# Kernel tuning notes

Hardware: AMD Instinct MI355X
Metric: run time of the kernel (lower is better)

Reference implementation:

```python
import jax, jax.numpy as jnp
import numpy as np

R = 32
EPS = 0.0
BN_EPS = 1e-5


def _voxelize(features, idx):
    # features: [C, N], idx: [N] int32 flat voxel index in [0, R^3)
    V = R * R * R
    pts = features.T  # [N, C]
    sums = jax.ops.segment_sum(pts, idx, num_segments=V)          # [V, C]
    cnts = jax.ops.segment_sum(jnp.ones_like(idx, jnp.float32), idx, num_segments=V)  # [V]
    avg = sums / jnp.maximum(cnts, 1.0)[:, None]
    mx = jax.ops.segment_max(pts, idx, num_segments=V)            # [V, C], -inf for empty
    mx = jnp.where(cnts[:, None] > 0, mx, 0.0)
    return avg, mx, cnts


def reference(features, coords, conv_w, conv_b, bn_gamma, bn_beta, bn_mean, bn_var):
    B, C, N = features.shape
    # --- coordinate normalization (coords detached in original) ---
    nc = coords - jnp.mean(coords, axis=2, keepdims=True)          # [B,3,N]
    norms = jnp.linalg.norm(nc, axis=1, keepdims=True)             # [B,1,N]
    denom = jnp.max(norms, axis=2, keepdims=True) * 2.0 + EPS      # [B,1,1]
    nc = nc / denom + 0.5
    nc = jnp.clip(nc * R, 0.0, R - 1)                              # [B,3,N]
    vox = jnp.round(nc).astype(jnp.int32)                          # [B,3,N]
    idx = vox[:, 0] * (R * R) + vox[:, 1] * R + vox[:, 2]          # [B,N]
    # --- dual scatter reduction (avg + max) per batch ---
    avg, mx, _ = jax.vmap(_voxelize)(features, idx)                # [B, V, C] each
    fea = jnp.concatenate([mx, avg], axis=-1)                      # [B, V, 2C]
    # --- 1x1 Conv3d == channel matmul ---
    y = jnp.einsum('bvc,oc->bvo', fea, conv_w) + conv_b            # [B, V, C]
    # --- BatchNorm3d (eval mode) ---
    y = (y - bn_mean) * (bn_gamma / jnp.sqrt(bn_var + BN_EPS)) + bn_beta
    # --- Swish ---
    y = y * jax.nn.sigmoid(y)
    out = jnp.transpose(y, (0, 2, 1)).reshape(B, C, R, R, R)
    return out, nc


def setup_inputs() -> dict:
    key = jax.random.key(0)
    ks = jax.random.split(key, 8)
    B, C, N = 8, 240, 16384
    return {
        'features': jax.random.normal(ks[0], (B, C, N), jnp.float32),
        'coords': jax.random.normal(ks[1], (B, 3, N), jnp.float32),
        'conv_w': jax.random.normal(ks[2], (C, 2 * C), jnp.float32) * 0.05,
        'conv_b': jax.random.normal(ks[3], (C,), jnp.float32) * 0.05,
        'bn_gamma': jnp.ones((C,), jnp.float32),
        'bn_beta': jnp.zeros((C,), jnp.float32),
        'bn_mean': jnp.zeros((C,), jnp.float32),
        'bn_var': jax.random.uniform(ks[4], (C,), jnp.float32, 0.5, 1.5),
    }
```

## Files before the change

kernel.cpp:

```cpp
#include <hip/hip_runtime.h>
#include <math.h>

#define RR 32
#define V 32768
#define C 240
#define N 16384
#define B 8
#define K2C 480
#define GZ 16
#define NGRP 2048
#define FPAD 488
#define EBUF 512

typedef __attribute__((ext_vector_type(8))) short bf16x8;
typedef __attribute__((ext_vector_type(4))) float f32x4;

__device__ __forceinline__ unsigned short f2bf(float x) {
    unsigned u = __float_as_uint(x);
    u += 0x7fffu + ((u >> 16) & 1u);
    return (unsigned short)(u >> 16);
}

__global__ __launch_bounds__(256) void prep_kernel(const float* __restrict__ feat,
                                                   unsigned short* __restrict__ featT,
                                                   const float* __restrict__ coords,
                                                   float* __restrict__ stats,
                                                   int* __restrict__ hist,
                                                   int* __restrict__ wlcnt,
                                                   const float* __restrict__ w,
                                                   unsigned short* __restrict__ w_bf) {
    __shared__ float t[C][33];
    int blk = blockIdx.x;
    int tid = threadIdx.x;
    if (blk < 4096) {
        int bx = blk & 511, b = blk >> 9;
        int n0 = bx * 32;
        int l = tid;
        const float* fb = feat + (size_t)b * C * N;
        unsigned short* fTb = featT + (size_t)b * N * C;
        int nl = l & 31, cs = l >> 5;
#pragma unroll
        for (int p = 0; p < 30; ++p) {
            int c = p * 8 + cs;
            t[c][nl] = fb[(size_t)c * N + n0 + nl];
        }
        __syncthreads();
        int ci = l & 127;
        int nh = l >> 7;
#pragma unroll
        for (int p = 0; p < 16; ++p) {
            int n = 2 * p + nh;
            if (ci < 120) {
                unsigned lo = f2bf(t[2 * ci][n]);
                unsigned hi = f2bf(t[2 * ci + 1][n]);
                *(unsigned*)&fTb[(size_t)(n0 + n) * C + 2 * ci] = lo | (hi << 16);
            }
        }
        return;
    }
    if (blk < 4352) {
        int tt = (blk - 4096) * 256 + tid;
        int4 z4 = {0, 0, 0, 0};
        ((int4*)hist)[tt] = z4;
        if (tt < 57600) {
            unsigned lo = f2bf(w[2 * tt]);
            unsigned hi = f2bf(w[2 * tt + 1]);
            ((unsigned*)w_bf)[tt] = lo | (hi << 16);
        }
        if (tt < B) wlcnt[tt] = 0;
        return;
    }
    int b = blk - 4352;
    const float* cb = coords + (size_t)b * 3 * N;
    __shared__ float red[256];
    float m[3];
    for (int d = 0; d < 3; ++d) {
        float s = 0.f;
        for (int n = tid; n < N; n += 256) s += cb[d * N + n];
        red[tid] = s; __syncthreads();
        for (int w2 = 128; w2 > 0; w2 >>= 1) { if (tid < w2) red[tid] += red[tid + w2]; __syncthreads(); }
        m[d] = red[0] / (float)N;
        __syncthreads();
    }
    float mx = 0.f;
    for (int n = tid; n < N; n += 256) {
        float dx = cb[0 * N + n] - m[0];
        float dy = cb[1 * N + n] - m[1];
        float dz = cb[2 * N + n] - m[2];
        mx = fmaxf(mx, dx * dx + dy * dy + dz * dz);
    }
    red[tid] = mx; __syncthreads();
    for (int w2 = 128; w2 > 0; w2 >>= 1) { if (tid < w2) red[tid] = fmaxf(red[tid], red[tid + w2]); __syncthreads(); }
    if (tid == 0) {
        stats[b * 4 + 0] = m[0];
        stats[b * 4 + 1] = m[1];
        stats[b * 4 + 2] = m[2];
        stats[b * 4 + 3] = 2.f * sqrtf(red[0]);
    }
}

__global__ __launch_bounds__(256) void nc_idx_kernel(const float* __restrict__ coords,
                                                     const float* __restrict__ stats,
                                                     float* __restrict__ nc_out,
                                                     int* __restrict__ idxbuf,
                                                     int* __restrict__ hist) {
    int t = blockIdx.x * 256 + threadIdx.x;
    int b = t >> 14;
    int n = t & (N - 1);
    float denom = stats[b * 4 + 3];
    int v[3];
#pragma unroll
    for (int d = 0; d < 3; ++d) {
        float x = coords[((size_t)b * 3 + d) * N + n];
        float t0 = (x - stats[b * 4 + d]) / denom + 0.5f;
        t0 = t0 * (float)RR;
        t0 = fminf(fmaxf(t0, 0.f), (float)(RR - 1));
        nc_out[((size_t)b * 3 + d) * N + n] = t0;
        v[d] = (int)rintf(t0);
    }
    int iv = v[0] * (RR * RR) + v[1] * RR + v[2];
    idxbuf[t] = iv;
    atomicAdd(hist + b * V + iv, 1);
}

__global__ __launch_bounds__(1024) void prefix_kernel(const int* __restrict__ hist,
                                                      int* __restrict__ starts,
                                                      int* __restrict__ cursor,
                                                      int* __restrict__ wl,
                                                      int* __restrict__ wlcnt) {
    __shared__ int part[1024];
    int b = blockIdx.x, t = threadIdx.x;
    int base = b * V + t * 32;
    const int4* hp = (const int4*)(hist + base);
    int4 h[8];
#pragma unroll
    for (int j = 0; j < 8; ++j) h[j] = hp[j];
    int pcA = h[0].x + h[0].y + h[0].z + h[0].w + h[1].x + h[1].y + h[1].z + h[1].w
            + h[2].x + h[2].y + h[2].z + h[2].w + h[3].x + h[3].y + h[3].z + h[3].w;
    int pcB = h[4].x + h[4].y + h[4].z + h[4].w + h[5].x + h[5].y + h[5].z + h[5].w
            + h[6].x + h[6].y + h[6].z + h[6].w + h[7].x + h[7].y + h[7].z + h[7].w;
    int s = pcA + pcB;
    if (pcA > 0) { int p = atomicAdd(wlcnt + b, 1); wl[b * NGRP + p] = 2 * t; }
    if (pcB > 0) { int p = atomicAdd(wlcnt + b, 1); wl[b * NGRP + p] = 2 * t + 1; }
    part[t] = s; __syncthreads();
    for (int off = 1; off < 1024; off <<= 1) {
        int x = (t >= off) ? part[t - off] : 0;
        __syncthreads();
        part[t] += x;
        __syncthreads();
    }
    int run = part[t] - s;
    int4* sp = (int4*)(starts + base);
    int4* cp = (int4*)(cursor + base);
#pragma unroll
    for (int j = 0; j < 8; ++j) {
        int4 o;
        o.x = run; run += h[j].x;
        o.y = run; run += h[j].y;
        o.z = run; run += h[j].z;
        o.w = run; run += h[j].w;
        sp[j] = o; cp[j] = o;
    }
}

__global__ __launch_bounds__(256) void plist_fill_kernel(const int* __restrict__ idxbuf,
                                                         int* __restrict__ cursor,
                                                         int* __restrict__ ptlist,
                                                         const int* __restrict__ hist,
                                                         const float* __restrict__ cbias,
                                                         const float* __restrict__ gamma,
                                                         const float* __restrict__ beta,
                                                         const float* __restrict__ mean,
                                                         const float* __restrict__ var,
                                                         float* __restrict__ out) {
    int blk = blockIdx.x;
    int tid = threadIdx.x;
    if (blk < 512) {
        int t = blk * 256 + tid;
        int b = t >> 14;
        int n = t & (N - 1);
        int iv = idxbuf[t];
        int pos = atomicAdd(cursor + b * V + iv, 1);
        ptlist[(b << 14) + pos] = (n << 5) | (iv & 31);
        return;
    }
    int blk2 = blk - 512;
    int b = blk2 >> 10, col = blk2 & 1023;
    int v0 = col * 32;
    __shared__ int hcol[32];
    if (tid < 32) hcol[tid] = hist[b * V + v0 + tid];
    __syncthreads();
    int pcA = 0, pcB = 0;
#pragma unroll
    for (int z = 0; z < 16; ++z) { pcA += hcol[z]; pcB += hcol[16 + z]; }
    if (pcA > 0 && pcB > 0) return;
    float* outb = out + (size_t)b * C * V;
    if (pcA == 0 && pcB == 0) {
        for (int i = tid; i < C * 8; i += 256) {
            int o = i >> 3, q = i & 7;
            float sc = gamma[o] * rsqrtf(var[o] + 1e-5f);
            float b0 = (cbias[o] - mean[o]) * sc + beta[o];
            float y = b0 / (1.f + __expf(-b0));
            float4 f4 = {y, y, y, y};
            *(float4*)&outb[(size_t)o * V + v0 + q * 4] = f4;
        }
        return;
    }
    int vh = (pcA == 0) ? v0 : v0 + 16;
    for (int i = tid; i < C * 4; i += 256) {
        int o = i >> 2, q = i & 3;
        float sc = gamma[o] * rsqrtf(var[o] + 1e-5f);
        float b0 = (cbias[o] - mean[o]) * sc + beta[o];
        float y = b0 / (1.f + __expf(-b0));
        float4 f4 = {y, y, y, y};
        *(float4*)&outb[(size_t)o * V + vh + q * 4] = f4;
    }
}

__global__ __launch_bounds__(256) void column_kernel(
    const unsigned short* __restrict__ featT,
    const int* __restrict__ ptlist,
    const int* __restrict__ starts,
    const int* __restrict__ hist,
    const unsigned short* __restrict__ w_bf,
    const float* __restrict__ cbias, const float* __restrict__ gamma,
    const float* __restrict__ beta, const float* __restrict__ mean,
    const float* __restrict__ var,
    const int* __restrict__ wl, const int* __restrict__ wlcnt,
    float* __restrict__ out) {
    const int bx = blockIdx.x, b = blockIdx.y;
    if (bx >= wlcnt[b]) return;
    const int g = wl[b * NGRP + bx];
    const int tid = threadIdx.x;
    const int v0 = g * GZ;
    float* outb = out + (size_t)b * C * V;

    __shared__ float A_s[C], B_s[C], rcp_s[GZ];
    __shared__ unsigned short fea_s[GZ][FPAD];
    __shared__ int cnt_s[GZ];
    __shared__ int ebuf[EBUF];

    if (tid < C) {
        float sc = gamma[tid] * rsqrtf(var[tid] + 1e-5f);
        A_s[tid] = sc;
        B_s[tid] = (cbias[tid] - mean[tid]) * sc + beta[tid];
    }
    if (tid < GZ) {
        int c0 = hist[b * V + v0 + tid];
        cnt_s[tid] = c0;
        rcp_s[tid] = 1.f / (float)max(c0, 1);
    }
    __syncthreads();

    int pc = 0;
#pragma unroll
    for (int z = 0; z < GZ; ++z) pc += cnt_s[z];

    for (int i = tid; i < GZ * FPAD / 2; i += 256) ((unsigned*)fea_s)[i] = 0u;

    const int c = tid;
    const bool act = tid < C;
    const int pos = starts[b * V + v0];
    const int* pl = ptlist + (b << 14) + pos;
    const unsigned short* fT = featT + (size_t)b * N * C;

    float s0 = 0.f, mx0 = -INFINITY;
    int curz = -1;
    for (int base = 0; base < pc; base += EBUF) {
        int mm = min(EBUF, pc - base);
        __syncthreads();
        for (int i = tid; i < mm; i += 256) ebuf[i] = pl[base + i];
        __syncthreads();
        if (act) {
            for (int i0 = 0; i0 < mm; i0 += 16) {
                int m = min(16, mm - i0);
                int e_[16];
#pragma unroll
                for (int j = 0; j < 16; ++j) e_[j] = ebuf[i0 + ((j < m) ? j : m - 1)];
                unsigned short u_[16];
#pragma unroll
                for (int j = 0; j < 16; ++j)
                    u_[j] = fT[(size_t)(e_[j] >> 5) * C + c];
#pragma unroll
                for (int j = 0; j < 16; ++j) {
                    if (j < m) {
                        int zj = e_[j] & (GZ - 1);
                        if (zj != curz) {
                            if (curz >= 0) {
                                fea_s[curz][c] = f2bf(mx0);
                                fea_s[curz][C + c] = f2bf(s0 * rcp_s[curz]);
                            }
                            curz = zj; s0 = 0.f; mx0 = -INFINITY;
                        }
                        float f = __uint_as_float(((unsigned)u_[j]) << 16);
                        s0 += f; mx0 = fmaxf(mx0, f);
                    }
                }
            }
        }
    }
    if (act && curz >= 0) {
        fea_s[curz][c] = f2bf(mx0);
        fea_s[curz][C + c] = f2bf(s0 * rcp_s[curz]);
    }
    __syncthreads();

    const int lane = tid & 63, wave = tid >> 6;
    const int mcnt = (wave == 3) ? 3 : 4;
    const int zl = lane & 15;
    const int koff = (lane >> 4) * 8;

    f32x4 acc[4];
#pragma unroll
    for (int i = 0; i < 4; ++i) acc[i] = (f32x4){0.f, 0.f, 0.f, 0.f};

#pragma unroll
    for (int kc = 0; kc < 15; ++kc) {
        const int kg = kc * 32 + koff;
        bf16x8 bfr = *(const bf16x8*)&fea_s[zl][kg];
        const unsigned short* wp = w_bf + (size_t)(wave * 64 + zl) * K2C + kg;
#pragma unroll
        for (int mt = 0; mt < 4; ++mt) {
            if (mt < mcnt) {
                bf16x8 afr = *(const bf16x8*)(wp + (size_t)mt * 16 * K2C);
                acc[mt] = __builtin_amdgcn_mfma_f32_16x16x32_bf16(afr, bfr, acc[mt], 0, 0, 0);
            }
        }
    }

    const int vv = v0 + zl;
    const int rbase = (lane >> 4) * 4;
#pragma unroll
    for (int mt = 0; mt < 4; ++mt) {
        if (mt < mcnt) {
#pragma unroll
            for (int r = 0; r < 4; ++r) {
                int o = (wave * 4 + mt) * 16 + rbase + r;
                float y = acc[mt][r] * A_s[o] + B_s[o];
                y = y / (1.f + __expf(-y));
                outb[(size_t)o * V + vv] = y;
            }
        }
    }
}

extern "C" void kernel_launch(void* const* d_in, const int* in_sizes, int n_in,
                              void* d_out, int out_size, void* d_ws, size_t ws_size,
                              hipStream_t stream) {
    const float* features = (const float*)d_in[0];
    const float* coords   = (const float*)d_in[1];
    const float* conv_w   = (const float*)d_in[2];
    const float* conv_b   = (const float*)d_in[3];
    const float* gamma    = (const float*)d_in[4];
    const float* beta     = (const float*)d_in[5];
    const float* mean     = (const float*)d_in[6];
    const float* var      = (const float*)d_in[7];

    float* out    = (float*)d_out;
    float* nc_out = out + (size_t)B * C * V;

    char* ws = (char*)d_ws;
    size_t off = 0;
    auto carve = [&](size_t bytes) { char* p = ws + off; off += (bytes + 255) & ~(size_t)255; return p; };
    int*            hist   = (int*)carve((size_t)B * V * 4);
    float*          stats  = (float*)carve(B * 4 * 4);
    int*            idxbuf = (int*)carve((size_t)B * N * 4);
    int*            starts = (int*)carve((size_t)B * V * 4);
    int*            cursor = (int*)carve((size_t)B * V * 4);
    int*            ptlist = (int*)carve((size_t)B * N * 4);
    int*            wl     = (int*)carve((size_t)B * NGRP * 4);
    int*            wlcnt  = (int*)carve((size_t)B * 4);
    unsigned short* w_bf   = (unsigned short*)carve((size_t)C * K2C * 2);
    unsigned short* featT  = (unsigned short*)carve((size_t)B * N * C * 2);
    (void)off;

    prep_kernel<<<4360, 256, 0, stream>>>(features, featT, coords, stats, hist, wlcnt, conv_w, w_bf);
    nc_idx_kernel<<<(B * N) / 256, 256, 0, stream>>>(coords, stats, nc_out, idxbuf, hist);
    prefix_kernel<<<B, 1024, 0, stream>>>(hist, starts, cursor, wl, wlcnt);
    plist_fill_kernel<<<512 + 1024 * B, 256, 0, stream>>>(idxbuf, cursor, ptlist, hist,
                                                          conv_b, gamma, beta, mean, var, out);
    column_kernel<<<dim3(NGRP, B), 256, 0, stream>>>(
        featT, ptlist, starts, hist, w_bf,
        conv_b, gamma, beta, mean, var, wl, wlcnt, out);
    (void)in_sizes; (void)n_in; (void)out_size;
}
```

Measured before the change: 614.4 us.

## Move empty-voxel fill into column kernel and double-buffer gather loads

The empty-group fill work leaves the plist kernel. prefix_kernel now records empty half-columns at the tail of each worklist, and column_kernel handles them with a constant-output branch. The plist kernel shrinks to just the scatter, and the 8192 mostly idle fill blocks go away. The gather loop in column_kernel now double-buffers its 16-element feature fetches to overlap load latency with the reduction, at the cost of more registers.

```diff
diff --git a/kernel.cpp b/kernel.cpp
--- a/kernel.cpp
+++ b/kernel.cpp
@@ -67,7 +67,7 @@
             unsigned hi = f2bf(w[2 * tt + 1]);
             ((unsigned*)w_bf)[tt] = lo | (hi << 16);
         }
-        if (tt < B) wlcnt[tt] = 0;
+        if (tt < 2 * B) wlcnt[tt] = 0;
         return;
     }
     int b = blk - 4352;
@@ -142,6 +142,9 @@
     int s = pcA + pcB;
     if (pcA > 0) { int p = atomicAdd(wlcnt + b, 1); wl[b * NGRP + p] = 2 * t; }
     if (pcB > 0) { int p = atomicAdd(wlcnt + b, 1); wl[b * NGRP + p] = 2 * t + 1; }
+    if (pcA == 0 && pcB == 0) { int q = atomicAdd(wlcnt + B + b, 1); wl[b * NGRP + NGRP - 1 - q] = (2 * t) | 0x10000; }
+    else if (pcA == 0)        { int q = atomicAdd(wlcnt + B + b, 1); wl[b * NGRP + NGRP - 1 - q] = 2 * t; }
+    else if (pcB == 0)        { int q = atomicAdd(wlcnt + B + b, 1); wl[b * NGRP + NGRP - 1 - q] = 2 * t + 1; }
     part[t] = s; __syncthreads();
     for (int off = 1; off < 1024; off <<= 1) {
         int x = (t >= off) ? part[t - off] : 0;
@@ -163,59 +166,48 @@
     }
 }
 
-__global__ __launch_bounds__(256) void plist_fill_kernel(const int* __restrict__ idxbuf,
-                                                         int* __restrict__ cursor,
-                                                         int* __restrict__ ptlist,
-                                                         const int* __restrict__ hist,
-                                                         const float* __restrict__ cbias,
-                                                         const float* __restrict__ gamma,
-                                                         const float* __restrict__ beta,
-                                                         const float* __restrict__ mean,
-                                                         const float* __restrict__ var,
-                                                         float* __restrict__ out) {
-    int blk = blockIdx.x;
-    int tid = threadIdx.x;
-    if (blk < 512) {
-        int t = blk * 256 + tid;
-        int b = t >> 14;
-        int n = t & (N - 1);
-        int iv = idxbuf[t];
-        int pos = atomicAdd(cursor + b * V + iv, 1);
-        ptlist[(b << 14) + pos] = (n << 5) | (iv & 31);
-        return;
-    }
-    int blk2 = blk - 512;
-    int b = blk2 >> 10, col = blk2 & 1023;
-    int v0 = col * 32;
-    __shared__ int hcol[32];
-    if (tid < 32) hcol[tid] = hist[b * V + v0 + tid];
-    __syncthreads();
-    int pcA = 0, pcB = 0;
-#pragma unroll
-    for (int z = 0; z < 16; ++z) { pcA += hcol[z]; pcB += hcol[16 + z]; }
-    if (pcA > 0 && pcB > 0) return;
-    float* outb = out + (size_t)b * C * V;
-    if (pcA == 0 && pcB == 0) {
-        for (int i = tid; i < C * 8; i += 256) {
-            int o = i >> 3, q = i & 7;
-            float sc = gamma[o] * rsqrtf(var[o] + 1e-5f);
-            float b0 = (cbias[o] - mean[o]) * sc + beta[o];
-            float y = b0 / (1.f + __expf(-b0));
-            float4 f4 = {y, y, y, y};
-            *(float4*)&outb[(size_t)o * V + v0 + q * 4] = f4;
-        }
-        return;
-    }
-    int vh = (pcA == 0) ? v0 : v0 + 16;
-    for (int i = tid; i < C * 4; i += 256) {
-        int o = i >> 2, q = i & 3;
-        float sc = gamma[o] * rsqrtf(var[o] + 1e-5f);
-        float b0 = (cbias[o] - mean[o]) * sc + beta[o];
-        float y = b0 / (1.f + __expf(-b0));
-        float4 f4 = {y, y, y, y};
-        *(float4*)&outb[(size_t)o * V + vh + q * 4] = f4;
-    }
-}
+__global__ __launch_bounds__(256) void plist_kernel(const int* __restrict__ idxbuf,
+                                                    int* __restrict__ cursor,
+                                                    int* __restrict__ ptlist) {
+    int t = blockIdx.x * 256 + threadIdx.x;
+    int b = t >> 14;
+    int n = t & (N - 1);
+    int iv = idxbuf[t];
+    int pos = atomicAdd(cursor + b * V + iv, 1);
+    ptlist[(b << 14) + pos] = (n << 5) | (iv & 31);
+}
+
+#define PREFETCH(U, Z0, Z1, basei)                                          \
+    {                                                                       \
+        Z0 = 0u; Z1 = 0u;                                                   \
+        _Pragma("unroll")                                                   \
+        for (int j = 0; j < 16; ++j) {                                      \
+            int idx = basei + j; idx = (idx < mm) ? idx : mm - 1;           \
+            int e = ebuf[idx];                                              \
+            U[j] = fT[(size_t)(e >> 5) * C + c];                            \
+            unsigned zz = (unsigned)(e & 15);                               \
+            if (j < 8) Z0 |= zz << (4 * j); else Z1 |= zz << (4 * (j - 8)); \
+        }                                                                   \
+    }
+
+#define PROCESS(U, Z0, Z1, basei)                                           \
+    {                                                                       \
+        _Pragma("unroll")                                                   \
+        for (int j = 0; j < 16; ++j) {                                      \
+            if (basei + j < mm) {                                           \
+                int zj = (int)(((j < 8 ? Z0 : Z1) >> (4 * (j & 7))) & 15u); \
+                if (zj != curz) {                                           \
+                    if (curz >= 0) {                                        \
+                        fea_s[curz][c] = f2bf(mx0);                         \
+                        fea_s[curz][C + c] = f2bf(s0 * rcp_s[curz]);        \
+                    }                                                       \
+                    curz = zj; s0 = 0.f; mx0 = -INFINITY;                   \
+                }                                                           \
+                float f = __uint_as_float(((unsigned)U[j]) << 16);          \
+                s0 += f; mx0 = fmaxf(mx0, f);                               \
+            }                                                               \
+        }                                                                   \
+    }
 
 __global__ __launch_bounds__(256) void column_kernel(
     const unsigned short* __restrict__ featT,
@@ -229,28 +221,54 @@
     const int* __restrict__ wl, const int* __restrict__ wlcnt,
     float* __restrict__ out) {
     const int bx = blockIdx.x, b = blockIdx.y;
-    if (bx >= wlcnt[b]) return;
-    const int g = wl[b * NGRP + bx];
+    const int nw = wlcnt[b];
+    const int ntot = nw + wlcnt[B + b];
+    if (bx >= ntot) return;
+    const bool isfill = (bx >= nw);
+    const int wle = isfill ? wl[b * NGRP + NGRP - 1 - (bx - nw)] : wl[b * NGRP + bx];
     const int tid = threadIdx.x;
-    const int v0 = g * GZ;
     float* outb = out + (size_t)b * C * V;
 
-    __shared__ float A_s[C], B_s[C], rcp_s[GZ];
+    __shared__ float A_s[C], B_s[C], y0_s[C], rcp_s[GZ];
     __shared__ unsigned short fea_s[GZ][FPAD];
     __shared__ int cnt_s[GZ];
     __shared__ int ebuf[EBUF];
 
+    const int g = wle & 0xffff;
+    const int v0 = g * GZ;
+
     if (tid < C) {
         float sc = gamma[tid] * rsqrtf(var[tid] + 1e-5f);
         A_s[tid] = sc;
-        B_s[tid] = (cbias[tid] - mean[tid]) * sc + beta[tid];
-    }
-    if (tid < GZ) {
+        float b0 = (cbias[tid] - mean[tid]) * sc + beta[tid];
+        B_s[tid] = b0;
+        y0_s[tid] = b0 / (1.f + __expf(-b0));
+    }
+    if (!isfill && tid < GZ) {
         int c0 = hist[b * V + v0 + tid];
         cnt_s[tid] = c0;
         rcp_s[tid] = 1.f / (float)max(c0, 1);
     }
     __syncthreads();
+
+    if (isfill) {
+        if (wle >> 16) {
+            for (int i = tid; i < C * 8; i += 256) {
+                int o = i >> 3, q = i & 7;
+                float y = y0_s[o];
+                float4 f4 = {y, y, y, y};
+                *(float4*)&outb[(size_t)o * V + v0 + q * 4] = f4;
+            }
+        } else {
+            for (int i = tid; i < C * 4; i += 256) {
+                int o = i >> 2, q = i & 3;
+                float y = y0_s[o];
+                float4 f4 = {y, y, y, y};
+                *(float4*)&outb[(size_t)o * V + v0 + q * 4] = f4;
+            }
+        }
+        return;
+    }
 
     int pc = 0;
 #pragma unroll
@@ -272,30 +290,14 @@
         for (int i = tid; i < mm; i += 256) ebuf[i] = pl[base + i];
         __syncthreads();
         if (act) {
-            for (int i0 = 0; i0 < mm; i0 += 16) {
-                int m = min(16, mm - i0);
-                int e_[16];
-#pragma unroll
-                for (int j = 0; j < 16; ++j) e_[j] = ebuf[i0 + ((j < m) ? j : m - 1)];
-                unsigned short u_[16];
-#pragma unroll
-                for (int j = 0; j < 16; ++j)
-                    u_[j] = fT[(size_t)(e_[j] >> 5) * C + c];
-#pragma unroll
-                for (int j = 0; j < 16; ++j) {
-                    if (j < m) {
-                        int zj = e_[j] & (GZ - 1);
-                        if (zj != curz) {
-                            if (curz >= 0) {
-                                fea_s[curz][c] = f2bf(mx0);
-                                fea_s[curz][C + c] = f2bf(s0 * rcp_s[curz]);
-                            }
-                            curz = zj; s0 = 0.f; mx0 = -INFINITY;
-                        }
-                        float f = __uint_as_float(((unsigned)u_[j]) << 16);
-                        s0 += f; mx0 = fmaxf(mx0, f);
-                    }
-                }
+            unsigned short uA[16], uB[16];
+            unsigned zA0 = 0, zA1 = 0, zB0 = 0, zB1 = 0;
+            PREFETCH(uA, zA0, zA1, 0);
+            for (int i0 = 0; i0 < mm; i0 += 32) {
+                if (i0 + 16 < mm) PREFETCH(uB, zB0, zB1, i0 + 16);
+                PROCESS(uA, zA0, zA1, i0);
+                if (i0 + 32 < mm) PREFETCH(uA, zA0, zA1, i0 + 32);
+                PROCESS(uB, zB0, zB1, i0 + 16);
             }
         }
     }
@@ -369,7 +371,7 @@
     int*            cursor = (int*)carve((size_t)B * V * 4);
     int*            ptlist = (int*)carve((size_t)B * N * 4);
     int*            wl     = (int*)carve((size_t)B * NGRP * 4);
-    int*            wlcnt  = (int*)carve((size_t)B * 4);
+    int*            wlcnt  = (int*)carve((size_t)2 * B * 4);
     unsigned short* w_bf   = (unsigned short*)carve((size_t)C * K2C * 2);
     unsigned short* featT  = (unsigned short*)carve((size_t)B * N * C * 2);
     (void)off;
@@ -377,8 +379,7 @@
     prep_kernel<<<4360, 256, 0, stream>>>(features, featT, coords, stats, hist, wlcnt, conv_w, w_bf);
     nc_idx_kernel<<<(B * N) / 256, 256, 0, stream>>>(coords, stats, nc_out, idxbuf, hist);
     prefix_kernel<<<B, 1024, 0, stream>>>(hist, starts, cursor, wl, wlcnt);
-    plist_fill_kernel<<<512 + 1024 * B, 256, 0, stream>>>(idxbuf, cursor, ptlist, hist,
-                                                          conv_b, gamma, beta, mean, var, out);
+    plist_kernel<<<(B * N) / 256, 256, 0, stream>>>(idxbuf, cursor, ptlist);
     column_kernel<<<dim3(NGRP, B), 256, 0, stream>>>(
         featT, ptlist, starts, hist, w_bf,
         conv_b, gamma, beta, mean, var, wl, wlcnt, out);
```

New measurement: 580.5 us. -5.5%, faster.
